# Performance work log

Measured on AMD Instinct MI355X. Metric: run time of the kernel, lower is better.

## Reference

```python
import jax, jax.numpy as jnp
import numpy as np
from jax import lax

K = 3
EPS = 1e-5


def get_graph_feature(x, k):
    # Faithful to the torch code, including flat .view() reshapes (no transpose)
    B, N = x.shape[0], x.shape[1]          # num_points = x.size(1)
    x = x.reshape(B, -1, N)                # (B, C, N) flat reshape
    C = x.shape[1]
    inner = -2.0 * jnp.einsum('bcn,bcm->bnm', x, x)           # (B, N, N)
    xx = jnp.sum(x * x, axis=1, keepdims=True)                # (B, 1, N)
    dist = -xx - inner - jnp.swapaxes(xx, 1, 2)               # neg sq distances
    idx = lax.top_k(dist, k)[1]                               # (B, N, k) nearest
    flat = x.reshape(B * N, C)                                # flat reshape (as torch .view)
    idx_full = (idx + (jnp.arange(B) * N)[:, None, None]).reshape(-1)
    feature = flat[idx_full].reshape(B, N, k, C)
    xc = x.reshape(B, N, 1, C)                                # flat reshape (as torch .view)
    feature = jnp.concatenate([feature - xc, jnp.broadcast_to(xc, (B, N, k, C))], axis=3)
    return feature.reshape(B, 2 * C, k, N)                    # flat reshape (as torch .view)


def bn(h, g, b, m, v, axis):
    shape = [1] * h.ndim
    shape[axis] = -1
    inv = g.reshape(shape) / jnp.sqrt(v.reshape(shape) + EPS)
    return (h - m.reshape(shape)) * inv + b.reshape(shape)


def setup_inputs() -> dict:
    key = jax.random.key(0)
    ks = jax.random.split(key, 24)
    B, N = 8, 4096

    def bn_params(i, c):
        return {
            f'bn{i}_g': jax.random.uniform(ks[4 * (ord(i) % 4)], (c,), jnp.float32) + 0.5,
            f'bn{i}_b': jax.random.normal(jax.random.fold_in(key, 10 + ord(i)), (c,), jnp.float32) * 0.1,
            f'bn{i}_m': jax.random.normal(jax.random.fold_in(key, 20 + ord(i)), (c,), jnp.float32) * 0.1,
            f'bn{i}_v': jax.random.uniform(jax.random.fold_in(key, 30 + ord(i)), (c,), jnp.float32) + 0.5,
        }

    inp = {
        'x': jax.random.normal(ks[0], (B, N, 3), jnp.float32),
        'w1': jax.random.normal(ks[1], (64, 6), jnp.float32) * (1.0 / np.sqrt(6.0)),
        'wA': jax.random.normal(ks[2], (256, 82), jnp.float32) * (1.0 / np.sqrt(82.0)),
        'bA': jax.random.normal(ks[3], (256,), jnp.float32) * 0.01,
        'wB': jax.random.normal(ks[4], (128, 256), jnp.float32) * (1.0 / np.sqrt(256.0)),
        'bB': jax.random.normal(ks[5], (128,), jnp.float32) * 0.01,
        'wC': jax.random.normal(ks[6], (3, 128), jnp.float32) * (1.0 / np.sqrt(128.0)),
        'bC': jax.random.normal(ks[7], (3,), jnp.float32) * 0.01,
    }
    inp.update(bn_params('1', 64))
    inp.update(bn_params('A', 256))
    inp.update(bn_params('B', 128))
    return inp


def reference(x, w1, wA, bA, wB, bB, wC, bC,
              bn1_g, bn1_b, bn1_m, bn1_v,
              bnA_g, bnA_b, bnA_m, bnA_v,
              bnB_g, bnB_b, bnB_m, bnB_v):
    f = get_graph_feature(x, K)                         # (B, 6, K, N)
    h = jnp.einsum('oc,bckn->bokn', w1, f)              # 1x1 conv, no bias
    h = jax.nn.leaky_relu(bn(h, bn1_g, bn1_b, bn1_m, bn1_v, 1), 0.2)
    x1 = jnp.max(h, axis=-1)                            # (B, 64, K)  (max over N!)
    x2 = jnp.max(get_graph_feature(x1, K), axis=-1)     # (B, 6, K)   (conv2 unused in source)
    x3 = jnp.max(get_graph_feature(x2, K), axis=-1)     # (B, 6, K)
    x4 = jnp.max(get_graph_feature(x3, K), axis=-1)     # (B, 6, K)
    xc = jnp.concatenate([x1, x2, x3, x4], axis=1)      # (B, 82, K)
    p = jnp.max(xc, axis=-1)                            # adaptive_max_pool1d -> (B, 82)
    h = jax.nn.leaky_relu(bn(p @ wA.T + bA, bnA_g, bnA_b, bnA_m, bnA_v, 1), 0.2)
    h = jax.nn.leaky_relu(bn(h @ wB.T + bB, bnB_g, bnB_b, bnB_m, bnB_v, 1), 0.2)
    return jax.nn.softmax(h @ wC.T + bC, axis=1)        # (B, 3)
```

## Files before the change

kernel.cpp:

```cpp
#include <hip/hip_runtime.h>
#include <math.h>

#define NPTS 4096
#define EPSV 1e-5f

template <int CTRL>
__device__ __forceinline__ float dpp_max(float v) {
#if __has_builtin(__builtin_amdgcn_update_dpp)
  int o = __builtin_amdgcn_update_dpp(0, __float_as_int(v), CTRL, 0xF, 0xF, true);
  return fmaxf(v, __int_as_float(o));
#else
  int lanemask = (CTRL == 0xB1) ? 1 : (CTRL == 0x4E) ? 2 : (CTRL == 0x141) ? 7 : 15;
  return fmaxf(v, __shfl_xor(v, lanemask, 16));
#endif
}

__global__ __launch_bounds__(512)
__attribute__((amdgpu_waves_per_eu(4, 4)))
void k_knn1(const float* __restrict__ x, int* __restrict__ idx1) {
  __shared__ float4 ppre[64];
  __shared__ float  scmax[64][32];
  __shared__ float2 thmask[65];
  __shared__ int    cnt[64];
  __shared__ float  candk[64][24];
  __shared__ int    candi[64][24];
  __shared__ float  dummy[512];
  const int b     = blockIdx.x >> 6;
  const int pr    = blockIdx.x & 63;
  const int pbase = pr * 64;
  const float* xb = x + b * (NPTS * 3);
  const int t = threadIdx.x;
  const int g = t >> 4;

  float q0x, q1x, q2x, q3x, q4x, q5x, q6x, q7x;
  float q0y, q1y, q2y, q3y, q4y, q5y, q6y, q7y;
  float q0z, q1z, q2z, q3z, q4z, q5z, q6z, q7z;
  {
    const float4* X = (const float4*)(xb + 8 * t);
    const float4* Y = (const float4*)(xb + NPTS + 8 * t);
    const float4* Z = (const float4*)(xb + 2 * NPTS + 8 * t);
    float4 x0 = X[0], x1 = X[1];
    float4 y0 = Y[0], y1 = Y[1];
    float4 z0 = Z[0], z1 = Z[1];
    q0x = x0.x; q1x = x0.y; q2x = x0.z; q3x = x0.w;
    q4x = x1.x; q5x = x1.y; q6x = x1.z; q7x = x1.w;
    q0y = y0.x; q1y = y0.y; q2y = y0.z; q3y = y0.w;
    q4y = y1.x; q5y = y1.y; q6y = y1.z; q7y = y1.w;
    q0z = z0.x; q1z = z0.y; q2z = z0.z; q3z = z0.w;
    q4z = z1.x; q5z = z1.y; q6z = z1.z; q7z = z1.w;
  }
  const float q0w = -fmaf(q0z, q0z, fmaf(q0y, q0y, q0x * q0x));
  const float q1w = -fmaf(q1z, q1z, fmaf(q1y, q1y, q1x * q1x));
  const float q2w = -fmaf(q2z, q2z, fmaf(q2y, q2y, q2x * q2x));
  const float q3w = -fmaf(q3z, q3z, fmaf(q3y, q3y, q3x * q3x));
  const float q4w = -fmaf(q4z, q4z, fmaf(q4y, q4y, q4x * q4x));
  const float q5w = -fmaf(q5z, q5z, fmaf(q5y, q5y, q5x * q5x));
  const float q6w = -fmaf(q6z, q6z, fmaf(q6y, q6y, q6x * q6x));
  const float q7w = -fmaf(q7z, q7z, fmaf(q7y, q7y, q7x * q7x));
  if (t < 64) {
    float px = xb[pbase + t];
    float py = xb[NPTS + pbase + t];
    float pz = xb[2 * NPTS + pbase + t];
    ppre[t] = make_float4(2.f * px, 2.f * py, 2.f * pz, 0.f);
    cnt[t] = 0;
  }
  __syncthreads();

  {
    float* wptr = ((t & 15) == 0) ? &scmax[0][g] : &dummy[t];
    const int wstep = ((t & 15) == 0) ? 32 : 0;
#pragma unroll 4
    for (int p = 0; p < 64; ++p) {
      float4 P = ppre[p];
      float k0 = fmaf(P.x, q0x, fmaf(P.y, q0y, fmaf(P.z, q0z, q0w)));
      float k1 = fmaf(P.x, q1x, fmaf(P.y, q1y, fmaf(P.z, q1z, q1w)));
      float k2 = fmaf(P.x, q2x, fmaf(P.y, q2y, fmaf(P.z, q2z, q2w)));
      float k3 = fmaf(P.x, q3x, fmaf(P.y, q3y, fmaf(P.z, q3z, q3w)));
      float k4 = fmaf(P.x, q4x, fmaf(P.y, q4y, fmaf(P.z, q4z, q4w)));
      float k5 = fmaf(P.x, q5x, fmaf(P.y, q5y, fmaf(P.z, q5z, q5w)));
      float k6 = fmaf(P.x, q6x, fmaf(P.y, q6y, fmaf(P.z, q6z, q6w)));
      float k7 = fmaf(P.x, q7x, fmaf(P.y, q7y, fmaf(P.z, q7z, q7w)));
      float v = fmaxf(fmaxf(fmaxf(k0, k1), fmaxf(k2, k3)),
                      fmaxf(fmaxf(k4, k5), fmaxf(k6, k7)));
      v = dpp_max<0xB1>(v);
      v = dpp_max<0x4E>(v);
      v = dpp_max<0x141>(v);
      v = dpp_max<0x140>(v);
      *wptr = v;
      wptr += wstep;
    }
  }
  __syncthreads();

  if (t < 64) {
    const float4* row = (const float4*)scmax[t];
    float4 r[8];
#pragma unroll
    for (int i = 0; i < 8; ++i) r[i] = row[i];
    float d0 = -INFINITY, d1 = -INFINITY, d2 = -INFINITY;
#pragma unroll
    for (int i = 0; i < 8; ++i) {
      float va[4] = {r[i].x, r[i].y, r[i].z, r[i].w};
#pragma unroll
      for (int u = 0; u < 4; ++u) {
        float v = va[u];
        float nd2 = fmaxf(d2, fminf(d1, v));
        float nd1 = fmaxf(d1, fminf(d0, v));
        d0 = fmaxf(d0, v); d1 = nd1; d2 = nd2;
      }
    }
    unsigned mask = 0;
#pragma unroll
    for (int i = 0; i < 8; ++i) {
      float va[4] = {r[i].x, r[i].y, r[i].z, r[i].w};
#pragma unroll
      for (int u = 0; u < 4; ++u)
        mask |= (va[u] >= d2) ? (1u << (4 * i + u)) : 0u;
    }
    thmask[t] = make_float2(d2, __uint_as_float(mask));
  } else if (t == 64) {
    thmask[64] = make_float2(0.f, 0.f);
  }
  __syncthreads();

  {
    float2 tm = thmask[0];
    for (int p = 0; p < 64; ++p) {
      float2 ntm = thmask[p + 1];
      unsigned mask = __float_as_uint(tm.y);
      if ((mask >> g) & 1u) {
        float th = tm.x;
        float4 P = ppre[p];
        float kk[8];
        kk[0] = fmaf(P.x, q0x, fmaf(P.y, q0y, fmaf(P.z, q0z, q0w)));
        kk[1] = fmaf(P.x, q1x, fmaf(P.y, q1y, fmaf(P.z, q1z, q1w)));
        kk[2] = fmaf(P.x, q2x, fmaf(P.y, q2y, fmaf(P.z, q2z, q2w)));
        kk[3] = fmaf(P.x, q3x, fmaf(P.y, q3y, fmaf(P.z, q3z, q3w)));
        kk[4] = fmaf(P.x, q4x, fmaf(P.y, q4y, fmaf(P.z, q4z, q4w)));
        kk[5] = fmaf(P.x, q5x, fmaf(P.y, q5y, fmaf(P.z, q5z, q5w)));
        kk[6] = fmaf(P.x, q6x, fmaf(P.y, q6y, fmaf(P.z, q6z, q6w)));
        kk[7] = fmaf(P.x, q7x, fmaf(P.y, q7y, fmaf(P.z, q7z, q7w)));
#pragma unroll
        for (int j = 0; j < 8; ++j) {
          if (kk[j] >= th) {
            int c = atomicAdd(&cnt[p], 1);
            if (c < 24) { candk[p][c] = kk[j]; candi[p][c] = 8 * t + j; }
          }
        }
      }
      tm = ntm;
    }
  }
  __syncthreads();

  if (t < 64) {
    int c = cnt[t]; if (c > 24) c = 24;
    int* op = idx1 + (b * NPTS + pbase + t) * 3;
    float pd = INFINITY; int pi = -1;
    for (int r = 0; r < 3; ++r) {
      float bd = -INFINITY; int bi = 0x7fffffff;
      for (int cc = 0; cc < c; ++cc) {
        float kv = candk[t][cc];
        int m = candi[t][cc];
        bool allowed = (kv < pd) || (kv == pd && m > pi);
        bool better  = (kv > bd) || (kv == bd && m < bi);
        if (allowed && better) { bd = kv; bi = m; }
      }
      op[r] = bi;
      pd = bd; pi = bi;
    }
  }
}

__global__ __launch_bounds__(256) void k_convmax(const float* __restrict__ x,
                                                 const int* __restrict__ idx1,
                                                 const float* __restrict__ w1,
                                                 float* __restrict__ pmax) {
  __shared__ float4 Ft4[128][2];
  __shared__ float  w1s[384];
  __shared__ float  smax[4][64];
  const int b    = blockIdx.x / 96;
  const int rr   = blockIdx.x - b * 96;
  const int kk   = rr >> 5;
  const int tile = rr & 31;
  const int t = threadIdx.x;
  for (int i = t; i < 384; i += 256) w1s[i] = w1[i];
  const float* xb = x + b * 12288;
  const int*   ib = idx1 + b * 12288;

  const int tn = t & 127, ch = t >> 7;
  const int n = tile * 128 + tn;
  float* ftrow = (float*)&Ft4[tn][0];
#pragma unroll
  for (int j = 0; j < 3; ++j) {
    int c = ch * 3 + j;
    int ofs = c * 12288 + kk * 4096 + n;
    int np  = ofs / 18;
    int rem = ofs - np * 18;
    int kp  = rem / 6;
    int cp  = rem - kp * 6;
    float val;
    if (cp < 3) {
      int jj = ib[np * 3 + kp];
      val = xb[jj * 3 + cp] - xb[np * 3 + cp];
    } else {
      val = xb[np * 3 + cp - 3];
    }
    ftrow[c] = val;
  }
  __syncthreads();

  const int o = t & 63, sub = t >> 6;
  float w[6];
#pragma unroll
  for (int c = 0; c < 6; ++c) w[c] = w1s[o * 6 + c];
  const int base = sub * 32;
  float mx = -INFINITY;

  float4 ra[4][2];
#pragma unroll
  for (int r = 0; r < 4; ++r) { ra[r][0] = Ft4[base + r][0]; ra[r][1] = Ft4[base + r][1]; }

  for (int i = 0; i < 32; i += 8) {
    float4 rb[4][2];
#pragma unroll
    for (int r = 0; r < 4; ++r) {
      rb[r][0] = Ft4[base + i + 4 + r][0];
      rb[r][1] = Ft4[base + i + 4 + r][1];
    }
#pragma unroll
    for (int r = 0; r < 4; ++r) {
      float h = w[0] * ra[r][0].x;
      h = fmaf(w[1], ra[r][0].y, h);
      h = fmaf(w[2], ra[r][0].z, h);
      h = fmaf(w[3], ra[r][0].w, h);
      h = fmaf(w[4], ra[r][1].x, h);
      h = fmaf(w[5], ra[r][1].y, h);
      mx = fmaxf(mx, h);
    }
#pragma unroll
    for (int r = 0; r < 4; ++r) {
      int nr = base + ((i + 8 + r) & 31);
      ra[r][0] = Ft4[nr][0]; ra[r][1] = Ft4[nr][1];
    }
#pragma unroll
    for (int r = 0; r < 4; ++r) {
      float h = w[0] * rb[r][0].x;
      h = fmaf(w[1], rb[r][0].y, h);
      h = fmaf(w[2], rb[r][0].z, h);
      h = fmaf(w[3], rb[r][0].w, h);
      h = fmaf(w[4], rb[r][1].x, h);
      h = fmaf(w[5], rb[r][1].y, h);
      mx = fmaxf(mx, h);
    }
  }
  smax[sub][o] = mx;
  __syncthreads();
  if (t < 64) {
    float m01 = fmaxf(smax[0][t], smax[1][t]);
    float m23 = fmaxf(smax[2][t], smax[3][t]);
    pmax[((b * 3 + kk) * 64 + t) * 32 + tile] = fmaxf(m01, m23);
  }
}

__device__ __forceinline__ void top3_insert(float d, int m,
                                            float& d0, float& d1, float& d2,
                                            int& i0, int& i1, int& i2) {
  if (d > d2) {
    bool g1 = d > d1;
    bool g0 = d > d0;
    d2 = g1 ? d1 : d;                 i2 = g1 ? i1 : m;
    d1 = g0 ? d0 : (g1 ? d : d1);     i1 = g0 ? i0 : (g1 ? m : i1);
    d0 = g0 ? d : d0;                 i0 = g0 ? m : i0;
  }
}

__global__ __launch_bounds__(256) void k_tail(
    const float* __restrict__ pmax,
    const float* __restrict__ bn1g, const float* __restrict__ bn1b,
    const float* __restrict__ bn1m, const float* __restrict__ bn1v,
    const float* __restrict__ wA, const float* __restrict__ bA,
    const float* __restrict__ bnAg, const float* __restrict__ bnAb,
    const float* __restrict__ bnAm, const float* __restrict__ bnAv,
    const float* __restrict__ wB, const float* __restrict__ bB,
    const float* __restrict__ bnBg, const float* __restrict__ bnBb,
    const float* __restrict__ bnBm, const float* __restrict__ bnBv,
    const float* __restrict__ wC, const float* __restrict__ bC,
    float* __restrict__ out) {
  __shared__ float a1[192];
  __shared__ int   idx2[192];
  __shared__ float a2[18], a3[18], a4[18];
  __shared__ int   idxs[18];
  __shared__ float pv[82];
  __shared__ float hA[256];
  __shared__ float hB[128];
  __shared__ float lg[3];
  const int b = blockIdx.x;
  const int t = threadIdx.x;

  if (t < 192) {
    int o = t / 3, k = t - o * 3;
    const float4* p4 = (const float4*)(pmax + ((b * 3 + k) * 64 + o) * 32);
    float4 v[8];
#pragma unroll
    for (int j = 0; j < 8; ++j) v[j] = p4[j];
    float mx = -INFINITY;
#pragma unroll
    for (int j = 0; j < 8; ++j) {
      mx = fmaxf(mx, fmaxf(fmaxf(v[j].x, v[j].y), fmaxf(v[j].z, v[j].w)));
    }
    float inv = bn1g[o] / sqrtf(bn1v[o] + EPSV);
    float val = (mx - bn1m[o]) * inv + bn1b[o];
    a1[o * 3 + k] = val >= 0.f ? val : 0.2f * val;
  }
  __syncthreads();

  if (t < 64) {
    float px = a1[t], py = a1[64 + t], pz = a1[128 + t];
    float pp = px * px; pp = fmaf(py, py, pp); pp = fmaf(pz, pz, pp);
    float d0 = -INFINITY, d1 = -INFINITY, d2 = -INFINITY;
    int i0 = 0, i1 = 0, i2 = 0;
#pragma unroll 8
    for (int m = 0; m < 64; ++m) {
      float qx = a1[m], qy = a1[64 + m], qz = a1[128 + m];
      float qq = qx * qx; qq = fmaf(qy, qy, qq); qq = fmaf(qz, qz, qq);
      float dot = px * qx; dot = fmaf(py, qy, dot); dot = fmaf(pz, qz, dot);
      float d = 2.f * dot - pp - qq;
      top3_insert(d, m, d0, d1, d2, i0, i1, i2);
    }
    idx2[t * 3 + 0] = i0; idx2[t * 3 + 1] = i1; idx2[t * 3 + 2] = i2;
  }
  __syncthreads();

  if (t < 18) {
    int o = t / 3, kk = t - o * 3;
    float mx = -INFINITY;
#pragma unroll 8
    for (int nn = 0; nn < 64; ++nn) {
      int ofs = o * 192 + kk * 64 + nn;
      int np = ofs / 18; int rem = ofs - np * 18;
      int kp = rem / 6;  int cp  = rem - kp * 6;
      float val = (cp < 3) ? (a1[idx2[np * 3 + kp] * 3 + cp] - a1[np * 3 + cp])
                           : a1[np * 3 + cp - 3];
      mx = fmaxf(mx, val);
    }
    a2[t] = mx;
  }
  __syncthreads();

  for (int stage = 0; stage < 2; ++stage) {
    const float* src = (stage == 0) ? a2 : a3;
    float*       dst = (stage == 0) ? a3 : a4;
    if (t < 6) {
      float px = src[t], py = src[6 + t], pz = src[12 + t];
      float pp = px * px; pp = fmaf(py, py, pp); pp = fmaf(pz, pz, pp);
      float d0 = -INFINITY, d1 = -INFINITY, d2 = -INFINITY;
      int i0 = 0, i1 = 0, i2 = 0;
#pragma unroll
      for (int m = 0; m < 6; ++m) {
        float qx = src[m], qy = src[6 + m], qz = src[12 + m];
        float qq = qx * qx; qq = fmaf(qy, qy, qq); qq = fmaf(qz, qz, qq);
        float dot = px * qx; dot = fmaf(py, qy, dot); dot = fmaf(pz, qz, dot);
        float d = 2.f * dot - pp - qq;
        top3_insert(d, m, d0, d1, d2, i0, i1, i2);
      }
      idxs[t * 3 + 0] = i0; idxs[t * 3 + 1] = i1; idxs[t * 3 + 2] = i2;
    }
    __syncthreads();
    if (t < 18) {
      int o = t / 3, kk = t - o * 3;
      float mx = -INFINITY;
#pragma unroll
      for (int nn = 0; nn < 6; ++nn) {
        int ofs = o * 18 + kk * 6 + nn;
        int np = ofs / 18; int rem = ofs - np * 18;
        int kp = rem / 6;  int cp  = rem - kp * 6;
        float val = (cp < 3) ? (src[idxs[np * 3 + kp] * 3 + cp] - src[np * 3 + cp])
                             : src[np * 3 + cp - 3];
        mx = fmaxf(mx, val);
      }
      dst[t] = mx;
    }
    __syncthreads();
  }

  if (t < 82) {
    float mx;
    if (t < 64)      { int o = t;      mx = fmaxf(fmaxf(a1[o*3], a1[o*3+1]), a1[o*3+2]); }
    else if (t < 70) { int o = t - 64; mx = fmaxf(fmaxf(a2[o*3], a2[o*3+1]), a2[o*3+2]); }
    else if (t < 76) { int o = t - 70; mx = fmaxf(fmaxf(a3[o*3], a3[o*3+1]), a3[o*3+2]); }
    else             { int o = t - 76; mx = fmaxf(fmaxf(a4[o*3], a4[o*3+1]), a4[o*3+2]); }
    pv[t] = mx;
  }
  __syncthreads();

  {
    float acc = bA[t];
    const float* wr = wA + t * 82;
#pragma unroll 8
    for (int i = 0; i < 82; ++i) acc = fmaf(wr[i], pv[i], acc);
    float inv = bnAg[t] / sqrtf(bnAv[t] + EPSV);
    float v = (acc - bnAm[t]) * inv + bnAb[t];
    hA[t] = v >= 0.f ? v : 0.2f * v;
  }
  __syncthreads();

  if (t < 128) {
    float acc = bB[t];
    const float4* wr4 = (const float4*)(wB + t * 256);
#pragma unroll 8
    for (int i = 0; i < 64; ++i) {
      float4 wv = wr4[i];
      acc = fmaf(wv.x, hA[4 * i + 0], acc);
      acc = fmaf(wv.y, hA[4 * i + 1], acc);
      acc = fmaf(wv.z, hA[4 * i + 2], acc);
      acc = fmaf(wv.w, hA[4 * i + 3], acc);
    }
    float inv = bnBg[t] / sqrtf(bnBv[t] + EPSV);
    float v = (acc - bnBm[t]) * inv + bnBb[t];
    hB[t] = v >= 0.f ? v : 0.2f * v;
  }
  __syncthreads();

  if (t < 3) {
    float acc = bC[t];
    const float* wr = wC + t * 128;
#pragma unroll 8
    for (int i = 0; i < 128; ++i) acc = fmaf(wr[i], hB[i], acc);
    lg[t] = acc;
  }
  __syncthreads();
  if (t == 0) {
    float m = fmaxf(fmaxf(lg[0], lg[1]), lg[2]);
    float e0 = expf(lg[0] - m), e1 = expf(lg[1] - m), e2 = expf(lg[2] - m);
    float s = e0 + e1 + e2;
    out[b * 3 + 0] = e0 / s;
    out[b * 3 + 1] = e1 / s;
    out[b * 3 + 2] = e2 / s;
  }
}

extern "C" void kernel_launch(void* const* d_in, const int* in_sizes, int n_in,
                              void* d_out, int out_size, void* d_ws, size_t ws_size,
                              hipStream_t stream) {
  (void)in_sizes; (void)n_in; (void)out_size; (void)ws_size;
  const float* x    = (const float*)d_in[0];
  const float* w1   = (const float*)d_in[1];
  const float* wA   = (const float*)d_in[2];
  const float* bA   = (const float*)d_in[3];
  const float* wB   = (const float*)d_in[4];
  const float* bB   = (const float*)d_in[5];
  const float* wC   = (const float*)d_in[6];
  const float* bC   = (const float*)d_in[7];
  const float* bn1g = (const float*)d_in[8];
  const float* bn1b = (const float*)d_in[9];
  const float* bn1m = (const float*)d_in[10];
  const float* bn1v = (const float*)d_in[11];
  const float* bnAg = (const float*)d_in[12];
  const float* bnAb = (const float*)d_in[13];
  const float* bnAm = (const float*)d_in[14];
  const float* bnAv = (const float*)d_in[15];
  const float* bnBg = (const float*)d_in[16];
  const float* bnBb = (const float*)d_in[17];
  const float* bnBm = (const float*)d_in[18];
  const float* bnBv = (const float*)d_in[19];
  float* out = (float*)d_out;

  int*   idx1 = (int*)d_ws;
  float* pmax = (float*)((char*)d_ws + 8 * 4096 * 3 * 4);

  k_knn1<<<512, 512, 0, stream>>>(x, idx1);
  k_convmax<<<768, 256, 0, stream>>>(x, idx1, w1, pmax);
  k_tail<<<8, 256, 0, stream>>>(pmax,
                                bn1g, bn1b, bn1m, bn1v,
                                wA, bA, bnAg, bnAb, bnAm, bnAv,
                                wB, bB, bnBg, bnBb, bnBm, bnBv,
                                wC, bC, out);
}
```

Before: 178.7 us.

## Double kNN block to 1024 threads with four candidates per thread

```diff
diff --git a/kernel.cpp b/kernel.cpp
--- a/kernel.cpp
+++ b/kernel.cpp
@@ -15,16 +15,15 @@
 #endif
 }
 
-__global__ __launch_bounds__(512)
-__attribute__((amdgpu_waves_per_eu(4, 4)))
+__global__ __launch_bounds__(1024)
 void k_knn1(const float* __restrict__ x, int* __restrict__ idx1) {
   __shared__ float4 ppre[64];
-  __shared__ float  scmax[64][32];
-  __shared__ float2 thmask[65];
+  __shared__ float  scmax[64 * 68];
+  __shared__ float4 thmask[65];
   __shared__ int    cnt[64];
   __shared__ float  candk[64][24];
   __shared__ int    candi[64][24];
-  __shared__ float  dummy[512];
+  __shared__ float  dummy[1024];
   const int b     = blockIdx.x >> 6;
   const int pr    = blockIdx.x & 63;
   const int pbase = pr * 64;
@@ -32,31 +31,14 @@
   const int t = threadIdx.x;
   const int g = t >> 4;
 
-  float q0x, q1x, q2x, q3x, q4x, q5x, q6x, q7x;
-  float q0y, q1y, q2y, q3y, q4y, q5y, q6y, q7y;
-  float q0z, q1z, q2z, q3z, q4z, q5z, q6z, q7z;
-  {
-    const float4* X = (const float4*)(xb + 8 * t);
-    const float4* Y = (const float4*)(xb + NPTS + 8 * t);
-    const float4* Z = (const float4*)(xb + 2 * NPTS + 8 * t);
-    float4 x0 = X[0], x1 = X[1];
-    float4 y0 = Y[0], y1 = Y[1];
-    float4 z0 = Z[0], z1 = Z[1];
-    q0x = x0.x; q1x = x0.y; q2x = x0.z; q3x = x0.w;
-    q4x = x1.x; q5x = x1.y; q6x = x1.z; q7x = x1.w;
-    q0y = y0.x; q1y = y0.y; q2y = y0.z; q3y = y0.w;
-    q4y = y1.x; q5y = y1.y; q6y = y1.z; q7y = y1.w;
-    q0z = z0.x; q1z = z0.y; q2z = z0.z; q3z = z0.w;
-    q4z = z1.x; q5z = z1.y; q6z = z1.z; q7z = z1.w;
-  }
-  const float q0w = -fmaf(q0z, q0z, fmaf(q0y, q0y, q0x * q0x));
-  const float q1w = -fmaf(q1z, q1z, fmaf(q1y, q1y, q1x * q1x));
-  const float q2w = -fmaf(q2z, q2z, fmaf(q2y, q2y, q2x * q2x));
-  const float q3w = -fmaf(q3z, q3z, fmaf(q3y, q3y, q3x * q3x));
-  const float q4w = -fmaf(q4z, q4z, fmaf(q4y, q4y, q4x * q4x));
-  const float q5w = -fmaf(q5z, q5z, fmaf(q5y, q5y, q5x * q5x));
-  const float q6w = -fmaf(q6z, q6z, fmaf(q6y, q6y, q6x * q6x));
-  const float q7w = -fmaf(q7z, q7z, fmaf(q7y, q7y, q7x * q7x));
+  float4 qx = *(const float4*)(xb + 4 * t);
+  float4 qy = *(const float4*)(xb + NPTS + 4 * t);
+  float4 qz = *(const float4*)(xb + 2 * NPTS + 4 * t);
+  float4 qw;
+  qw.x = -fmaf(qz.x, qz.x, fmaf(qy.x, qy.x, qx.x * qx.x));
+  qw.y = -fmaf(qz.y, qz.y, fmaf(qy.y, qy.y, qx.y * qx.y));
+  qw.z = -fmaf(qz.z, qz.z, fmaf(qy.z, qy.z, qx.z * qx.z));
+  qw.w = -fmaf(qz.w, qz.w, fmaf(qy.w, qy.w, qx.w * qx.w));
   if (t < 64) {
     float px = xb[pbase + t];
     float py = xb[NPTS + pbase + t];
@@ -67,21 +49,16 @@
   __syncthreads();
 
   {
-    float* wptr = ((t & 15) == 0) ? &scmax[0][g] : &dummy[t];
-    const int wstep = ((t & 15) == 0) ? 32 : 0;
+    float* wptr = ((t & 15) == 0) ? &scmax[g] : &dummy[t];
+    const int wstep = ((t & 15) == 0) ? 68 : 0;
 #pragma unroll 4
     for (int p = 0; p < 64; ++p) {
       float4 P = ppre[p];
-      float k0 = fmaf(P.x, q0x, fmaf(P.y, q0y, fmaf(P.z, q0z, q0w)));
-      float k1 = fmaf(P.x, q1x, fmaf(P.y, q1y, fmaf(P.z, q1z, q1w)));
-      float k2 = fmaf(P.x, q2x, fmaf(P.y, q2y, fmaf(P.z, q2z, q2w)));
-      float k3 = fmaf(P.x, q3x, fmaf(P.y, q3y, fmaf(P.z, q3z, q3w)));
-      float k4 = fmaf(P.x, q4x, fmaf(P.y, q4y, fmaf(P.z, q4z, q4w)));
-      float k5 = fmaf(P.x, q5x, fmaf(P.y, q5y, fmaf(P.z, q5z, q5w)));
-      float k6 = fmaf(P.x, q6x, fmaf(P.y, q6y, fmaf(P.z, q6z, q6w)));
-      float k7 = fmaf(P.x, q7x, fmaf(P.y, q7y, fmaf(P.z, q7z, q7w)));
-      float v = fmaxf(fmaxf(fmaxf(k0, k1), fmaxf(k2, k3)),
-                      fmaxf(fmaxf(k4, k5), fmaxf(k6, k7)));
+      float k0 = fmaf(P.x, qx.x, fmaf(P.y, qy.x, fmaf(P.z, qz.x, qw.x)));
+      float k1 = fmaf(P.x, qx.y, fmaf(P.y, qy.y, fmaf(P.z, qz.y, qw.y)));
+      float k2 = fmaf(P.x, qx.z, fmaf(P.y, qy.z, fmaf(P.z, qz.z, qw.z)));
+      float k3 = fmaf(P.x, qx.w, fmaf(P.y, qy.w, fmaf(P.z, qz.w, qw.w)));
+      float v = fmaxf(fmaxf(k0, k1), fmaxf(k2, k3));
       v = dpp_max<0xB1>(v);
       v = dpp_max<0x4E>(v);
       v = dpp_max<0x141>(v);
@@ -93,14 +70,12 @@
   __syncthreads();
 
   if (t < 64) {
-    const float4* row = (const float4*)scmax[t];
-    float4 r[8];
-#pragma unroll
-    for (int i = 0; i < 8; ++i) r[i] = row[i];
+    const float4* row = (const float4*)&scmax[t * 68];
     float d0 = -INFINITY, d1 = -INFINITY, d2 = -INFINITY;
 #pragma unroll
-    for (int i = 0; i < 8; ++i) {
-      float va[4] = {r[i].x, r[i].y, r[i].z, r[i].w};
+    for (int i = 0; i < 16; ++i) {
+      float4 r = row[i];
+      float va[4] = {r.x, r.y, r.z, r.w};
 #pragma unroll
       for (int u = 0; u < 4; ++u) {
         float v = va[u];
@@ -109,44 +84,45 @@
         d0 = fmaxf(d0, v); d1 = nd1; d2 = nd2;
       }
     }
-    unsigned mask = 0;
+    unsigned lo = 0, hi = 0;
 #pragma unroll
     for (int i = 0; i < 8; ++i) {
-      float va[4] = {r[i].x, r[i].y, r[i].z, r[i].w};
-#pragma unroll
-      for (int u = 0; u < 4; ++u)
-        mask |= (va[u] >= d2) ? (1u << (4 * i + u)) : 0u;
-    }
-    thmask[t] = make_float2(d2, __uint_as_float(mask));
+      float4 r = row[i];
+      float va[4] = {r.x, r.y, r.z, r.w};
+#pragma unroll
+      for (int u = 0; u < 4; ++u) lo |= (va[u] >= d2) ? (1u << (4 * i + u)) : 0u;
+    }
+#pragma unroll
+    for (int i = 8; i < 16; ++i) {
+      float4 r = row[i];
+      float va[4] = {r.x, r.y, r.z, r.w};
+#pragma unroll
+      for (int u = 0; u < 4; ++u) hi |= (va[u] >= d2) ? (1u << (4 * (i - 8) + u)) : 0u;
+    }
+    thmask[t] = make_float4(d2, __uint_as_float(lo), __uint_as_float(hi), 0.f);
   } else if (t == 64) {
-    thmask[64] = make_float2(0.f, 0.f);
+    thmask[64] = make_float4(0.f, 0.f, 0.f, 0.f);
   }
   __syncthreads();
 
   {
-    float2 tm = thmask[0];
+    const unsigned gbit = g & 31;
+    const bool ghi = (g >= 32);
+    float4 tm = thmask[0];
     for (int p = 0; p < 64; ++p) {
-      float2 ntm = thmask[p + 1];
-      unsigned mask = __float_as_uint(tm.y);
-      if ((mask >> g) & 1u) {
+      float4 ntm = thmask[p + 1];
+      unsigned mw = __float_as_uint(ghi ? tm.z : tm.y);
+      if ((mw >> gbit) & 1u) {
         float th = tm.x;
         float4 P = ppre[p];
-        float kk[8];
-        kk[0] = fmaf(P.x, q0x, fmaf(P.y, q0y, fmaf(P.z, q0z, q0w)));
-        kk[1] = fmaf(P.x, q1x, fmaf(P.y, q1y, fmaf(P.z, q1z, q1w)));
-        kk[2] = fmaf(P.x, q2x, fmaf(P.y, q2y, fmaf(P.z, q2z, q2w)));
-        kk[3] = fmaf(P.x, q3x, fmaf(P.y, q3y, fmaf(P.z, q3z, q3w)));
-        kk[4] = fmaf(P.x, q4x, fmaf(P.y, q4y, fmaf(P.z, q4z, q4w)));
-        kk[5] = fmaf(P.x, q5x, fmaf(P.y, q5y, fmaf(P.z, q5z, q5w)));
-        kk[6] = fmaf(P.x, q6x, fmaf(P.y, q6y, fmaf(P.z, q6z, q6w)));
-        kk[7] = fmaf(P.x, q7x, fmaf(P.y, q7y, fmaf(P.z, q7z, q7w)));
-#pragma unroll
-        for (int j = 0; j < 8; ++j) {
-          if (kk[j] >= th) {
-            int c = atomicAdd(&cnt[p], 1);
-            if (c < 24) { candk[p][c] = kk[j]; candi[p][c] = 8 * t + j; }
-          }
-        }
+        float k0 = fmaf(P.x, qx.x, fmaf(P.y, qy.x, fmaf(P.z, qz.x, qw.x)));
+        float k1 = fmaf(P.x, qx.y, fmaf(P.y, qy.y, fmaf(P.z, qz.y, qw.y)));
+        float k2 = fmaf(P.x, qx.z, fmaf(P.y, qy.z, fmaf(P.z, qz.z, qw.z)));
+        float k3 = fmaf(P.x, qx.w, fmaf(P.y, qy.w, fmaf(P.z, qz.w, qw.w)));
+        if (k0 >= th) { int c = atomicAdd(&cnt[p], 1); if (c < 24) { candk[p][c] = k0; candi[p][c] = 4 * t + 0; } }
+        if (k1 >= th) { int c = atomicAdd(&cnt[p], 1); if (c < 24) { candk[p][c] = k1; candi[p][c] = 4 * t + 1; } }
+        if (k2 >= th) { int c = atomicAdd(&cnt[p], 1); if (c < 24) { candk[p][c] = k2; candi[p][c] = 4 * t + 2; } }
+        if (k3 >= th) { int c = atomicAdd(&cnt[p], 1); if (c < 24) { candk[p][c] = k3; candi[p][c] = 4 * t + 3; } }
       }
       tm = ntm;
     }
@@ -469,7 +445,7 @@
   int*   idx1 = (int*)d_ws;
   float* pmax = (float*)((char*)d_ws + 8 * 4096 * 3 * 4);
 
-  k_knn1<<<512, 512, 0, stream>>>(x, idx1);
+  k_knn1<<<512, 1024, 0, stream>>>(x, idx1);
   k_convmax<<<768, 256, 0, stream>>>(x, idx1, w1, pmax);
   k_tail<<<8, 256, 0, stream>>>(pmax,
                                 bn1g, bn1b, bn1m, bn1v,
```

Result: slower. 196.2 us (+9.8%).
